# Kernel tuning notes

Measured on AMD Instinct MI355X. Metric: run time of the kernel, lower is better.

The kernel has to match this reference:

```python
import jax, jax.numpy as jnp
import numpy as np

NUM_CODES = 8192
CODE_DIM = 512
B, H, W = 16, 32, 32


def setup_inputs() -> dict:
    key = jax.random.key(0)
    k1, k2 = jax.random.split(key)
    z_e = jax.random.normal(k1, (B, H, W, CODE_DIM), dtype=jnp.float32)
    # variance_scaling(1.0, 'fan_in', 'uniform') ~ U(-sqrt(3/fan_in), sqrt(3/fan_in))
    lim = np.sqrt(3.0 / CODE_DIM)
    codebook = jax.random.uniform(k2, (NUM_CODES, CODE_DIM), dtype=jnp.float32,
                                  minval=-lim, maxval=lim)
    return {"z_e": z_e, "codebook": codebook}


def reference(z_e, codebook):
    shape = z_e.shape
    num_codes, code_dim = codebook.shape
    flat = z_e.reshape(-1, code_dim)                       # [N, D]
    d = (jnp.sum(flat * flat, axis=1, keepdims=True)
         + jnp.sum(codebook * codebook, axis=1)
         - 2.0 * jnp.matmul(flat, codebook.T))             # [N, K]
    indices = jnp.argmin(d, axis=1)                        # [N]
    z_q = codebook[indices].reshape(shape)
    idx_out = indices.reshape(shape[:-1])
    commitment_loss = jnp.mean((jax.lax.stop_gradient(z_q) - z_e) ** 2)
    codebook_loss = jnp.mean((z_q - jax.lax.stop_gradient(z_e)) ** 2)
    z_q_st = z_e + jax.lax.stop_gradient(z_q - z_e)        # straight-through
    # perplexity: mean one-hot == normalized histogram (avoids NxK one-hot)
    n = flat.shape[0]
    counts = jnp.zeros((num_codes,), dtype=z_e.dtype).at[indices].add(1.0)
    avg_probs = counts / n
    perplexity = jnp.exp(-jnp.sum(avg_probs * jnp.log(avg_probs + 1e-10)))
    return (z_q_st, idx_out, commitment_loss, codebook_loss, perplexity)
```

## Files before the change

kernel.cpp:

```cpp
#include <hip/hip_runtime.h>


#define N_PTS   16384
#define DIM     512
#define K_CODES 8192
#define KB      512
#define NSPLIT  16
#define OUT0_N  (N_PTS * DIM)
#define NELEM_F (8388608.0f)
#define MARGIN  1.5e-2f

typedef _Float16 half8 __attribute__((ext_vector_type(8)));
typedef _Float16 f16x4 __attribute__((ext_vector_type(4)));
typedef float    f32x4 __attribute__((ext_vector_type(4)));

#define SZ_A3    (16384UL * 512 * 2)
#define SZ_B3    (8192UL * 512 * 2)
#define OFF_A3   0UL
#define OFF_B3   (OFF_A3 + SZ_A3)
#define OFF_CN   (OFF_B3 + SZ_B3)
#define OFF_PV1  (OFF_CN + 32768UL)
#define SZ_P     (16UL * 16384 * 4)
#define OFF_PI1  (OFF_PV1 + SZ_P)
#define OFF_PV2  (OFF_PI1 + SZ_P)
#define OFF_PI2  (OFF_PV2 + SZ_P)
#define OFF_PSUM (OFF_PI2 + SZ_P)
#define OFF_CNT  (OFF_PSUM + 65536UL)
#define WS_NEED  (OFF_CNT + 32768UL)

#define GLOAD_LDS16(g, l) \
    __builtin_amdgcn_global_load_lds( \
        (const __attribute__((address_space(1))) unsigned int*)(g), \
        (__attribute__((address_space(3))) unsigned int*)(l), 16, 0, 0)

__global__ __launch_bounds__(128) void prep_all(const float* __restrict__ z_e,
                                                const float* __restrict__ cb,
                                                _Float16* __restrict__ A3,
                                                _Float16* __restrict__ B3,
                                                float* __restrict__ cnorm,
                                                unsigned int* __restrict__ counts) {
    const int b = blockIdx.x;
    const int t = threadIdx.x;
    if (b < 64) counts[b * 128 + t] = 0u;
    if (b < N_PTS) {
        const long r = b;
        const int d = t * 4;
        const float4 v = *(const float4*)(z_e + r * DIM + d);
        f16x4 h;
        h[0] = (_Float16)v.x; h[1] = (_Float16)v.y;
        h[2] = (_Float16)v.z; h[3] = (_Float16)v.w;
        *(f16x4*)(A3 + r * 512 + d) = h;
    } else {
        const long r = b - N_PTS;
        const int d = t * 4;
        const float4 v = *(const float4*)(cb + r * DIM + d);
        f16x4 h;
        h[0] = (_Float16)v.x; h[1] = (_Float16)v.y;
        h[2] = (_Float16)v.z; h[3] = (_Float16)v.w;
        *(f16x4*)(B3 + r * 512 + d) = h;
        float s = v.x * v.x + v.y * v.y + v.z * v.z + v.w * v.w;
#pragma unroll
        for (int o = 32; o > 0; o >>= 1) s += __shfl_down(s, o, 64);
        __shared__ float red[2];
        if ((t & 63) == 0) red[t >> 6] = s;
        __syncthreads();
        if (t == 0) cnorm[r] = red[0] + red[1];
    }
}

__global__ __launch_bounds__(128) void cnorm_kernel(const float* __restrict__ cb,
                                                    float* __restrict__ cnorm) {
    const int k = blockIdx.x;
    const int t = threadIdx.x;
    const float4 v = *(const float4*)(cb + (size_t)k * DIM + t * 4);
    float s = v.x * v.x + v.y * v.y + v.z * v.z + v.w * v.w;
#pragma unroll
    for (int o = 32; o > 0; o >>= 1) s += __shfl_down(s, o, 64);
    __shared__ float red[2];
    if ((t & 63) == 0) red[t >> 6] = s;
    __syncthreads();
    if (t == 0) cnorm[k] = red[0] + red[1];
}

__global__ __launch_bounds__(256, 3) void score_kernel(
    const _Float16* __restrict__ A3, const _Float16* __restrict__ B3,
    const float* __restrict__ cnorm,
    float* __restrict__ pv1, int* __restrict__ pi1,
    float* __restrict__ pv2, int* __restrict__ pi2) {
    __shared__ _Float16 As[128 * 64];
    __shared__ _Float16 Bs[128 * 64];
    __shared__ float mv1[128][2], mv2[128][2];
    __shared__ int   mj1[128][2], mj2[128][2];

    const int tid = threadIdx.x;
    const int w = tid >> 6;
    const int l = tid & 63;
    const int pbase = blockIdx.x * 128;
    const int nsplit = blockIdx.y;
    const int wmb = (w >> 1) * 64;
    const int wnb = (w & 1) * 64;
    const int srow = w * 8 + (l >> 3);
    const int scolh = (((l & 7) ^ ((l >> 3) & 7)) * 8);

    const _Float16* aB[4];
    const _Float16* bR[4];
#pragma unroll
    for (int it = 0; it < 4; ++it) {
        aB[it] = A3 + (long)(pbase + it * 32 + srow) * 512 + scolh;
        bR[it] = B3 + (long)(it * 32 + srow) * 512 + scolh;
    }

    const int q = l >> 4, x7 = l & 7, m16 = l & 15;
    const int koff0 = ((q ^ x7) * 8);
    const int rowAf = (wmb + m16) * 64;
    const int rowBf = (wnb + m16) * 64;

    float v1[16], v2[16];
    int i12[16];
#pragma unroll
    for (int s = 0; s < 16; ++s) { v1[s] = 3.0e38f; v2[s] = 3.0e38f; i12[s] = 0; }

#pragma unroll 1
    for (int nt = 0; nt < 4; ++nt) {
        const int kbase = nsplit * 512 + nt * 128;
        const long bOff = (long)kbase * 512;
        f32x4 acc[4][4];
#pragma unroll
        for (int mi = 0; mi < 4; ++mi)
#pragma unroll
            for (int ni = 0; ni < 4; ++ni)
                acc[mi][ni] = (f32x4){0.f, 0.f, 0.f, 0.f};

#pragma unroll 1
        for (int kt = 0; kt < KB / 64; ++kt) {
            const long ka = (long)kt * 64;
            __syncthreads();
#pragma unroll
            for (int it = 0; it < 4; ++it)
                GLOAD_LDS16(aB[it] + ka, &As[it * 2048 + w * 512]);
#pragma unroll
            for (int it = 0; it < 4; ++it)
                GLOAD_LDS16(bR[it] + bOff + ka, &Bs[it * 2048 + w * 512]);
            __syncthreads();
#pragma unroll
            for (int ks = 0; ks < 2; ++ks) {
                const int ko = koff0 ^ (ks * 32);
                half8 af[4], bf[4];
#pragma unroll
                for (int mi = 0; mi < 4; ++mi)
                    af[mi] = *(half8*)&As[rowAf + mi * 1024 + ko];
#pragma unroll
                for (int ni = 0; ni < 4; ++ni)
                    bf[ni] = *(half8*)&Bs[rowBf + ni * 1024 + ko];
#pragma unroll
                for (int mi = 0; mi < 4; ++mi)
#pragma unroll
                    for (int ni = 0; ni < 4; ++ni)
                        acc[mi][ni] = __builtin_amdgcn_mfma_f32_16x16x32_f16(
                            af[mi], bf[ni], acc[mi][ni], 0, 0, 0);
            }
        }
#pragma unroll
        for (int ni = 0; ni < 4; ++ni) {
            const int k = kbase + wnb + ni * 16 + m16;
            const float cn = cnorm[k];
#pragma unroll
            for (int mi = 0; mi < 4; ++mi)
#pragma unroll
                for (int r = 0; r < 4; ++r) {
                    const float s = fmaf(-2.0f, acc[mi][ni][r], cn);
                    const int slot = mi * 4 + r;
                    if (s < v1[slot]) {
                        v2[slot] = v1[slot];
                        i12[slot] = (k << 16) | (i12[slot] >> 16);
                        v1[slot] = s;
                    } else if (s < v2[slot]) {
                        v2[slot] = s;
                        i12[slot] = (i12[slot] & 0xffff0000) | k;
                    }
                }
        }
    }

#pragma unroll
    for (int slot = 0; slot < 16; ++slot) {
        float a1 = v1[slot], a2 = v2[slot];
        int b1 = i12[slot] >> 16, b2 = i12[slot] & 0xffff;
#pragma unroll
        for (int m = 1; m < 16; m <<= 1) {
            const float c1 = __shfl_xor(a1, m, 64);
            const int   d1 = __shfl_xor(b1, m, 64);
            const float c2 = __shfl_xor(a2, m, 64);
            const int   d2 = __shfl_xor(b2, m, 64);
            if (c1 < a1 || (c1 == a1 && d1 < b1)) {
                if (a1 < c2 || (a1 == c2 && b1 < d2)) { a2 = a1; b2 = b1; }
                else { a2 = c2; b2 = d2; }
                a1 = c1; b1 = d1;
            } else {
                if (c1 < a2 || (c1 == a2 && d1 < b2)) { a2 = c1; b2 = d1; }
            }
        }
        if ((l & 15) == 0) {
            const int sm = slot >> 2, sr = slot & 3;
            const int pr = wmb + sm * 16 + (l >> 4) * 4 + sr;
            const int h = w & 1;
            mv1[pr][h] = a1; mj1[pr][h] = b1;
            mv2[pr][h] = a2; mj2[pr][h] = b2;
        }
    }
    __syncthreads();
    if (tid < 128) {
        float a1 = mv1[tid][0], a2 = mv2[tid][0];
        int b1 = mj1[tid][0], b2 = mj2[tid][0];
        const float c1 = mv1[tid][1], c2 = mv2[tid][1];
        const int   d1 = mj1[tid][1], d2 = mj2[tid][1];
        if (c1 < a1 || (c1 == a1 && d1 < b1)) {
            if (a1 < c2 || (a1 == c2 && b1 < d2)) { a2 = a1; b2 = b1; }
            else { a2 = c2; b2 = d2; }
            a1 = c1; b1 = d1;
        } else {
            if (c1 < a2 || (c1 == a2 && d1 < b2)) { a2 = c1; b2 = d1; }
        }
        const size_t o = (size_t)nsplit * N_PTS + pbase + tid;
        pv1[o] = a1; pi1[o] = b1; pv2[o] = a2; pi2[o] = b2;
    }
}

__global__ __launch_bounds__(128) void gather_kernel(
    const float* __restrict__ z_e, const float* __restrict__ cb,
    const float* __restrict__ pv1, const int* __restrict__ pi1,
    const float* __restrict__ pv2, const int* __restrict__ pi2,
    float* __restrict__ out_q, float* __restrict__ out_idx,
    unsigned int* __restrict__ counts, float* __restrict__ psums) {
    const int p = blockIdx.x;
    const int t = threadIdx.x;

    __shared__ float sv1[NSPLIT], sv2[NSPLIT];
    __shared__ int   si1[NSPLIT], si2[NSPLIT];
    if (t < NSPLIT) {
        const size_t o = (size_t)t * N_PTS + p;
        sv1[t] = pv1[o]; si1[t] = pi1[o];
        sv2[t] = pv2[o]; si2[t] = pi2[o];
    }
    __syncthreads();

    float bv = 3.0e38f; int bi = 0x7fffffff;
#pragma unroll
    for (int s = 0; s < NSPLIT; ++s) {
        const float v = sv1[s];
        const int i = si1[s];
        if (v < bv || (v == bv && i < bi)) { bv = v; bi = i; }
    }
    float second = 3.0e38f;
    int cand[8]; int nc = 1; cand[0] = bi;
#pragma unroll
    for (int s = 0; s < NSPLIT; ++s) {
        const float v = sv1[s];
        const int i = si1[s];
        const float w2 = sv2[s];
        const int j = si2[s];
        if (i != bi) {
            if (v < second) second = v;
            if (v <= bv + MARGIN && nc < 8) cand[nc++] = i;
        }
        if (j != bi) {
            if (w2 < second) second = w2;
            if (w2 <= bv + MARGIN && nc < 8) cand[nc++] = j;
        }
    }

    __shared__ double dred[2];
    if (second - bv <= MARGIN && nc > 1) {
        double bestv = 1.0e300; int besti = 0x7fffffff;
        for (int c = 0; c < nc; ++c) {
            const int k = cand[c];
            double part = 0.0;
#pragma unroll
            for (int j = 0; j < 4; ++j) {
                const int d = t * 4 + j;
                const double cv = (double)cb[(size_t)k * DIM + d];
                const double zv = (double)z_e[(size_t)p * DIM + d];
                part += cv * cv - 2.0 * zv * cv;
            }
#pragma unroll
            for (int o = 32; o > 0; o >>= 1) part += __shfl_down(part, o, 64);
            if ((t & 63) == 0) dred[t >> 6] = part;
            __syncthreads();
            const double s = dred[0] + dred[1];
            __syncthreads();
            if (s < bestv || (s == bestv && k < besti)) { bestv = s; besti = k; }
        }
        bi = besti;
    }

    const float4 z = *(const float4*)(z_e + (size_t)p * DIM + t * 4);
    const float4 c = *(const float4*)(cb + (size_t)bi * DIM + t * 4);
    float4 d, o;
    d.x = c.x - z.x; d.y = c.y - z.y; d.z = c.z - z.z; d.w = c.w - z.w;
    o.x = z.x + d.x; o.y = z.y + d.y; o.z = z.z + d.z; o.w = z.w + d.w;
    *(float4*)(out_q + (size_t)p * DIM + t * 4) = o;
    float ls = d.x * d.x + d.y * d.y + d.z * d.z + d.w * d.w;
#pragma unroll
    for (int off = 32; off > 0; off >>= 1) ls += __shfl_down(ls, off, 64);
    __shared__ float red[2];
    if ((t & 63) == 0) red[t >> 6] = ls;
    __syncthreads();
    if (t == 0) {
        psums[p] = red[0] + red[1];
        out_idx[p] = (float)bi;
        atomicAdd(&counts[bi], 1u);
    }
}

__global__ __launch_bounds__(256) void finalize_kernel(
    const unsigned int* __restrict__ counts, const float* __restrict__ psums,
    float* __restrict__ out_scalars) {
    const int t = threadIdx.x;
    float ent = 0.0f;
    for (int b = t; b < K_CODES; b += 256) {
        const float pr = (float)counts[b] * (1.0f / 16384.0f);
        ent += pr * logf(pr + 1e-10f);
    }
    float ss = 0.0f;
    for (int i = t; i < N_PTS; i += 256) ss += psums[i];
#pragma unroll
    for (int off = 32; off > 0; off >>= 1) {
        ent += __shfl_down(ent, off, 64);
        ss += __shfl_down(ss, off, 64);
    }
    __shared__ float re[4], rs[4];
    if ((t & 63) == 0) { re[t >> 6] = ent; rs[t >> 6] = ss; }
    __syncthreads();
    if (t == 0) {
        const float loss = (rs[0] + rs[1] + rs[2] + rs[3]) * (1.0f / NELEM_F);
        out_scalars[0] = loss;
        out_scalars[1] = loss;
        out_scalars[2] = expf(-(re[0] + re[1] + re[2] + re[3]));
    }
}

#define FB_SPLIT 4
#define FB_KS    (K_CODES / FB_SPLIT)
#define FB_MT    128
#define FB_KT    128
#define FB_DT    32
#define FB_PITCH 36

__global__ __launch_bounds__(256, 2) void fb_dist_argmin_kernel(
    const float* __restrict__ z_e, const float* __restrict__ cb,
    const float* __restrict__ cnorm,
    float* __restrict__ pmin, int* __restrict__ pidx) {
    __shared__ float xs[FB_MT * FB_PITCH];
    __shared__ float cs[FB_KT * FB_PITCH];
    const int tid = threadIdx.x;
    const int tx = tid & 15, ty = tid >> 4;
    const int pbase = blockIdx.x * FB_MT;
    const int kbase0 = blockIdx.y * FB_KS;
    const int scol = (tid & 7) * 4, srow0 = tid >> 3;
    float mn[8], acc[8][8];
    int mi[8];
#pragma unroll
    for (int i = 0; i < 8; ++i) { mn[i] = 3.0e38f; mi[i] = 0; }
    for (int kt = 0; kt < FB_KS / FB_KT; ++kt) {
        const int kbase = kbase0 + kt * FB_KT;
#pragma unroll
        for (int i = 0; i < 8; ++i)
#pragma unroll
            for (int j = 0; j < 8; ++j) acc[i][j] = 0.0f;
        for (int dc = 0; dc < DIM / FB_DT; ++dc) {
            const int dbase = dc * FB_DT;
            __syncthreads();
#pragma unroll
            for (int it = 0; it < 4; ++it) {
                const int row = srow0 + it * 32;
                *(float4*)(xs + row * FB_PITCH + scol) =
                    *(const float4*)(z_e + (size_t)(pbase + row) * DIM + dbase + scol);
                *(float4*)(cs + row * FB_PITCH + scol) =
                    *(const float4*)(cb + (size_t)(kbase + row) * DIM + dbase + scol);
            }
            __syncthreads();
#pragma unroll 2
            for (int dd = 0; dd < FB_DT; dd += 4) {
                float4 xv[8], cv[8];
#pragma unroll
                for (int i = 0; i < 8; ++i)
                    xv[i] = *(const float4*)(xs + (ty + 16 * i) * FB_PITCH + dd);
#pragma unroll
                for (int j = 0; j < 8; ++j)
                    cv[j] = *(const float4*)(cs + (tx + 16 * j) * FB_PITCH + dd);
#pragma unroll
                for (int i = 0; i < 8; ++i)
#pragma unroll
                    for (int j = 0; j < 8; ++j)
                        acc[i][j] += xv[i].x * cv[j].x + xv[i].y * cv[j].y +
                                     xv[i].z * cv[j].z + xv[i].w * cv[j].w;
            }
        }
#pragma unroll
        for (int j = 0; j < 8; ++j) {
            const int k = kbase + tx + 16 * j;
            const float cn = cnorm[k];
#pragma unroll
            for (int i = 0; i < 8; ++i) {
                const float s = cn - 2.0f * acc[i][j];
                if (s < mn[i]) { mn[i] = s; mi[i] = k; }
            }
        }
    }
    float* rmin = xs;
    int* ridx = (int*)cs;
    __syncthreads();
#pragma unroll
    for (int i = 0; i < 8; ++i) {
        const int p = ty + 16 * i;
        rmin[p * 16 + tx] = mn[i];
        ridx[p * 16 + tx] = mi[i];
    }
    __syncthreads();
    if (tid < FB_MT) {
        float best = rmin[tid * 16];
        int bi = ridx[tid * 16];
#pragma unroll
        for (int t = 1; t < 16; ++t) {
            const float v = rmin[tid * 16 + t];
            const int k2 = ridx[tid * 16 + t];
            if (v < best || (v == best && k2 < bi)) { best = v; bi = k2; }
        }
        pmin[(size_t)blockIdx.y * N_PTS + pbase + tid] = best;
        pidx[(size_t)blockIdx.y * N_PTS + pbase + tid] = bi;
    }
}

__global__ __launch_bounds__(128) void fb_gather_kernel(
    const float* __restrict__ z_e, const float* __restrict__ cb,
    const float* __restrict__ pmin, const int* __restrict__ pidx,
    float* __restrict__ out_q, float* __restrict__ out_idx,
    unsigned int* __restrict__ counts, float* __restrict__ psums) {
    const int p = blockIdx.x;
    const int t = threadIdx.x;
    float best = pmin[p];
    int bi = pidx[p];
#pragma unroll
    for (int s = 1; s < FB_SPLIT; ++s) {
        const float v = pmin[(size_t)s * N_PTS + p];
        const int k2 = pidx[(size_t)s * N_PTS + p];
        if (v < best || (v == best && k2 < bi)) { best = v; bi = k2; }
    }
    const float4 z = *(const float4*)(z_e + (size_t)p * DIM + t * 4);
    const float4 c = *(const float4*)(cb + (size_t)bi * DIM + t * 4);
    float4 d, o;
    d.x = c.x - z.x; d.y = c.y - z.y; d.z = c.z - z.z; d.w = c.w - z.w;
    o.x = z.x + d.x; o.y = z.y + d.y; o.z = z.z + d.z; o.w = z.w + d.w;
    *(float4*)(out_q + (size_t)p * DIM + t * 4) = o;
    float ls = d.x * d.x + d.y * d.y + d.z * d.z + d.w * d.w;
#pragma unroll
    for (int off = 32; off > 0; off >>= 1) ls += __shfl_down(ls, off, 64);
    __shared__ float red[2];
    if ((t & 63) == 0) red[t >> 6] = ls;
    __syncthreads();
    if (t == 0) {
        psums[p] = red[0] + red[1];
        out_idx[p] = (float)bi;
        atomicAdd(&counts[bi], 1u);
    }
}

extern "C" void kernel_launch(void* const* d_in, const int* in_sizes, int n_in,
                              void* d_out, int out_size, void* d_ws, size_t ws_size,
                              hipStream_t stream) {
    const float* z_e = (const float*)d_in[0];
    const float* cb  = (const float*)d_in[1];
    float* out = (float*)d_out;
    char* ws = (char*)d_ws;

    if (ws_size >= WS_NEED) {
        _Float16* A3      = (_Float16*)(ws + OFF_A3);
        _Float16* B3      = (_Float16*)(ws + OFF_B3);
        float* cnorm      = (float*)(ws + OFF_CN);
        float* pv1        = (float*)(ws + OFF_PV1);
        int* pi1          = (int*)(ws + OFF_PI1);
        float* pv2        = (float*)(ws + OFF_PV2);
        int* pi2          = (int*)(ws + OFF_PI2);
        float* psums      = (float*)(ws + OFF_PSUM);
        unsigned int* cnt = (unsigned int*)(ws + OFF_CNT);

        prep_all<<<N_PTS + K_CODES, 128, 0, stream>>>(z_e, cb, A3, B3, cnorm, cnt);
        dim3 g(N_PTS / 128, NSPLIT);
        score_kernel<<<g, 256, 0, stream>>>(A3, B3, cnorm, pv1, pi1, pv2, pi2);
        gather_kernel<<<N_PTS, 128, 0, stream>>>(z_e, cb, pv1, pi1, pv2, pi2,
                                                 out, out + OUT0_N, cnt, psums);
        finalize_kernel<<<1, 256, 0, stream>>>(cnt, psums, out + OUT0_N + N_PTS);
    } else {
        float* cnorm      = (float*)ws;
        float* pmin       = (float*)(ws + 32768);
        int* pidx         = (int*)(ws + 32768 + 262144);
        unsigned int* cnt = (unsigned int*)(ws + 32768 + 2 * 262144);
        float* psums      = (float*)(ws + 32768 + 2 * 262144 + 32768);

        hipMemsetAsync(cnt, 0, 32768, stream);
        cnorm_kernel<<<K_CODES, 128, 0, stream>>>(cb, cnorm);
        dim3 grid1(N_PTS / FB_MT, FB_SPLIT);
        fb_dist_argmin_kernel<<<grid1, 256, 0, stream>>>(z_e, cb, cnorm, pmin, pidx);
        fb_gather_kernel<<<N_PTS, 128, 0, stream>>>(z_e, cb, pmin, pidx,
                                                    out, out + OUT0_N, cnt, psums);
        finalize_kernel<<<1, 256, 0, stream>>>(cnt, psums, out + OUT0_N + N_PTS);
    }
}
```

Measured before the change: 368.2 us.

## Rewrite score GEMM as 256x256 double-buffered, phase-interleaved MFMA pipeline

The fp16 distance GEMM moves from 128x128 tiles with 256 threads and single-buffered LDS to 256x256 tiles with 512 threads and a 128 KB double-buffered LDS. Global-to-LDS loads for the next K step are split across four compute phases, with explicit vmcnt waits, barriers and setprio around the MFMA bursts. The aim is to hide load latency behind compute and to raise data reuse per tile. The top-2 argmin is reduced per 256-code tile across lanes and waves, then merged into a running result. The large shared-memory footprint limits occupancy, and the hand-written waitcnt and barrier schedule is fragile.

```diff
diff --git a/kernel.cpp b/kernel.cpp
--- a/kernel.cpp
+++ b/kernel.cpp
@@ -4,7 +4,6 @@
 #define N_PTS   16384
 #define DIM     512
 #define K_CODES 8192
-#define KB      512
 #define NSPLIT  16
 #define OUT0_N  (N_PTS * DIM)
 #define NELEM_F (8388608.0f)
@@ -82,148 +81,188 @@
     if (t == 0) cnorm[k] = red[0] + red[1];
 }
 
-__global__ __launch_bounds__(256, 3) void score_kernel(
+__device__ __forceinline__ void top2_merge(float& a1, int& b1, float& a2, int& b2,
+                                           const float c1, const int d1,
+                                           const float c2, const int d2) {
+    if (c1 < a1 || (c1 == a1 && d1 < b1)) {
+        if (a1 < c2 || (a1 == c2 && b1 < d2)) { a2 = a1; b2 = b1; }
+        else { a2 = c2; b2 = d2; }
+        a1 = c1; b1 = d1;
+    } else {
+        if (c1 < a2 || (c1 == a2 && d1 < b2)) { a2 = c1; b2 = d1; }
+    }
+}
+
+__global__ __launch_bounds__(512, 2) void score_kernel(
     const _Float16* __restrict__ A3, const _Float16* __restrict__ B3,
     const float* __restrict__ cnorm,
     float* __restrict__ pv1, int* __restrict__ pi1,
     float* __restrict__ pv2, int* __restrict__ pi2) {
-    __shared__ _Float16 As[128 * 64];
-    __shared__ _Float16 Bs[128 * 64];
-    __shared__ float mv1[128][2], mv2[128][2];
-    __shared__ int   mj1[128][2], mj2[128][2];
+    __shared__ _Float16 smem[65536];
 
     const int tid = threadIdx.x;
-    const int w = tid >> 6;
-    const int l = tid & 63;
-    const int pbase = blockIdx.x * 128;
+    const int w   = tid >> 6;
+    const int l   = tid & 63;
+    const int wm  = w >> 2;
+    const int wn  = w & 3;
+    const int m16 = l & 15;
+    const int qq  = l >> 4;
+    const int x7  = l & 7;
+    const int pbase  = blockIdx.x * 256;
     const int nsplit = blockIdx.y;
-    const int wmb = (w >> 1) * 64;
-    const int wnb = (w & 1) * 64;
-    const int srow = w * 8 + (l >> 3);
-    const int scolh = (((l & 7) ^ ((l >> 3) & 7)) * 8);
-
-    const _Float16* aB[4];
-    const _Float16* bR[4];
-#pragma unroll
-    for (int it = 0; it < 4; ++it) {
-        aB[it] = A3 + (long)(pbase + it * 32 + srow) * 512 + scolh;
-        bR[it] = B3 + (long)(it * 32 + srow) * 512 + scolh;
-    }
-
-    const int q = l >> 4, x7 = l & 7, m16 = l & 15;
-    const int koff0 = ((q ^ x7) * 8);
-    const int rowAf = (wmb + m16) * 64;
-    const int rowBf = (wnb + m16) * 64;
-
-    float v1[16], v2[16];
-    int i12[16];
-#pragma unroll
-    for (int s = 0; s < 16; ++s) { v1[s] = 3.0e38f; v2[s] = 3.0e38f; i12[s] = 0; }
+
+    const int srow = tid >> 3;
+    const int sc   = ((tid & 7) ^ (srow & 7)) * 8;
+    const _Float16* gA = A3 + (size_t)(pbase + srow) * 512 + sc;
+
+    const int rA = wm * 128 + m16;
+    const int rB = wn * 64  + m16;
+    const int k0 = (qq ^ x7) * 8;
+
+#define STAGE_A(q, tau) \
+    GLOAD_LDS16(gA + (q) * 64 * 512 + (tau) * 64, \
+                &smem[(((tau) & 1) * 32768) + (q) * 4096 + w * 512])
+#define STAGE_B(q, tau) \
+    GLOAD_LDS16(gB + (q) * 64 * 512 + (tau) * 64, \
+                &smem[(((tau) & 1) * 32768) + 16384 + (q) * 4096 + w * 512])
+
+#define PHASE(mh, nh, STAGE_STMT, VM_STMT) do {                                 \
+    half8 af[4][2]; half8 bf[2][2];                                             \
+    _Pragma("unroll")                                                           \
+    for (int i_ = 0; i_ < 4; ++i_) {                                            \
+        const int r_ = (rA + ((mh) * 4 + i_) * 16) * 64;                        \
+        af[i_][0] = *(const half8*)&smem[bufo + r_ + k0];                       \
+        af[i_][1] = *(const half8*)&smem[bufo + r_ + (k0 ^ 32)];                \
+    }                                                                           \
+    _Pragma("unroll")                                                           \
+    for (int j_ = 0; j_ < 2; ++j_) {                                            \
+        const int r_ = (rB + ((nh) * 2 + j_) * 16) * 64;                        \
+        bf[j_][0] = *(const half8*)&smem[bufo + 16384 + r_ + k0];               \
+        bf[j_][1] = *(const half8*)&smem[bufo + 16384 + r_ + (k0 ^ 32)];        \
+    }                                                                           \
+    STAGE_STMT;                                                                 \
+    __builtin_amdgcn_s_barrier();                                               \
+    asm volatile("s_waitcnt lgkmcnt(0)" ::: "memory");                          \
+    __builtin_amdgcn_sched_barrier(0);                                          \
+    __builtin_amdgcn_s_setprio(1);                                              \
+    _Pragma("unroll")                                                           \
+    for (int i_ = 0; i_ < 4; ++i_)                                              \
+        _Pragma("unroll")                                                       \
+        for (int j_ = 0; j_ < 2; ++j_) {                                        \
+            acc[(mh) * 4 + i_][(nh) * 2 + j_] =                                 \
+                __builtin_amdgcn_mfma_f32_16x16x32_f16(                         \
+                    af[i_][0], bf[j_][0], acc[(mh) * 4 + i_][(nh) * 2 + j_],    \
+                    0, 0, 0);                                                   \
+            acc[(mh) * 4 + i_][(nh) * 2 + j_] =                                 \
+                __builtin_amdgcn_mfma_f32_16x16x32_f16(                         \
+                    af[i_][1], bf[j_][1], acc[(mh) * 4 + i_][(nh) * 2 + j_],    \
+                    0, 0, 0);                                                   \
+        }                                                                       \
+    __builtin_amdgcn_s_setprio(0);                                              \
+    VM_STMT;                                                                    \
+    __builtin_amdgcn_s_barrier();                                               \
+    __builtin_amdgcn_sched_barrier(0);                                          \
+} while (0)
+
+    float rv1 = 3.0e38f, rv2 = 3.0e38f;
+    int   ri1 = 0x7fffffff, ri2 = 0x7fffffff;
+
+    float* sc1 = (float*)smem;
+    float* sc2 = sc1 + 1024;
+    int*   si1 = (int*)(sc2 + 1024);
+    int*   si2 = si1 + 1024;
 
 #pragma unroll 1
-    for (int nt = 0; nt < 4; ++nt) {
-        const int kbase = nsplit * 512 + nt * 128;
-        const long bOff = (long)kbase * 512;
-        f32x4 acc[4][4];
-#pragma unroll
-        for (int mi = 0; mi < 4; ++mi)
+    for (int nt = 0; nt < 2; ++nt) {
+        const int kbase = nsplit * 512 + nt * 256;
+        const _Float16* gB = B3 + (size_t)(kbase + srow) * 512 + sc;
+
+        f32x4 acc[8][4];
+#pragma unroll
+        for (int mi = 0; mi < 8; ++mi)
 #pragma unroll
             for (int ni = 0; ni < 4; ++ni)
                 acc[mi][ni] = (f32x4){0.f, 0.f, 0.f, 0.f};
 
+        STAGE_A(0, 0); STAGE_A(2, 0); STAGE_A(1, 0); STAGE_A(3, 0);
+        STAGE_B(0, 0); STAGE_B(1, 0); STAGE_B(2, 0); STAGE_B(3, 0);
+        STAGE_A(0, 1); STAGE_A(2, 1);
+        asm volatile("s_waitcnt vmcnt(2)" ::: "memory");
+        __builtin_amdgcn_s_barrier();
+        __builtin_amdgcn_sched_barrier(0);
+
 #pragma unroll 1
-        for (int kt = 0; kt < KB / 64; ++kt) {
-            const long ka = (long)kt * 64;
-            __syncthreads();
-#pragma unroll
-            for (int it = 0; it < 4; ++it)
-                GLOAD_LDS16(aB[it] + ka, &As[it * 2048 + w * 512]);
-#pragma unroll
-            for (int it = 0; it < 4; ++it)
-                GLOAD_LDS16(bR[it] + bOff + ka, &Bs[it * 2048 + w * 512]);
-            __syncthreads();
-#pragma unroll
-            for (int ks = 0; ks < 2; ++ks) {
-                const int ko = koff0 ^ (ks * 32);
-                half8 af[4], bf[4];
-#pragma unroll
-                for (int mi = 0; mi < 4; ++mi)
-                    af[mi] = *(half8*)&As[rowAf + mi * 1024 + ko];
-#pragma unroll
-                for (int ni = 0; ni < 4; ++ni)
-                    bf[ni] = *(half8*)&Bs[rowBf + ni * 1024 + ko];
-#pragma unroll
-                for (int mi = 0; mi < 4; ++mi)
-#pragma unroll
-                    for (int ni = 0; ni < 4; ++ni)
-                        acc[mi][ni] = __builtin_amdgcn_mfma_f32_16x16x32_f16(
-                            af[mi], bf[ni], acc[mi][ni], 0, 0, 0);
+        for (int g = 0; g < 8; ++g) {
+            const int bufo = (g & 1) * 32768;
+            PHASE(0, 0,
+                  { if (g < 7) { STAGE_A(1, g + 1); STAGE_A(3, g + 1); } },
+                  {});
+            PHASE(0, 1,
+                  { if (g < 7) { STAGE_B(0, g + 1); STAGE_B(1, g + 1); } },
+                  {});
+            PHASE(1, 0,
+                  { if (g < 7) { STAGE_B(2, g + 1); STAGE_B(3, g + 1); } },
+                  {});
+            PHASE(1, 1,
+                  { if (g < 6) { STAGE_A(0, g + 2); STAGE_A(2, g + 2); } },
+                  { if (g < 6) asm volatile("s_waitcnt vmcnt(2)" ::: "memory");
+                    else if (g == 6) asm volatile("s_waitcnt vmcnt(0)" ::: "memory"); });
+        }
+
+        const int kb2 = kbase + wn * 64;
+        float cn[4];
+#pragma unroll
+        for (int ni = 0; ni < 4; ++ni) cn[ni] = cnorm[kb2 + ni * 16 + m16];
+
+#pragma unroll
+        for (int mi = 0; mi < 8; ++mi) {
+#pragma unroll
+            for (int r = 0; r < 4; ++r) {
+                float a1 = 3.0e38f, a2 = 3.0e38f;
+                int   b1 = 0x7fffffff, b2 = 0x7fffffff;
+#pragma unroll
+                for (int ni = 0; ni < 4; ++ni) {
+                    const float s = fmaf(-2.0f, acc[mi][ni][r], cn[ni]);
+                    const int k = kb2 + ni * 16 + m16;
+                    if (s < a1) { a2 = a1; b2 = b1; a1 = s; b1 = k; }
+                    else if (s < a2) { a2 = s; b2 = k; }
+                }
+#pragma unroll
+                for (int m = 1; m < 16; m <<= 1) {
+                    const float c1 = __shfl_xor(a1, m, 64);
+                    const int   d1 = __shfl_xor(b1, m, 64);
+                    const float c2 = __shfl_xor(a2, m, 64);
+                    const int   d2 = __shfl_xor(b2, m, 64);
+                    top2_merge(a1, b1, a2, b2, c1, d1, c2, d2);
+                }
+                if ((l & 15) == 0) {
+                    const int pr = wm * 128 + mi * 16 + qq * 4 + r;
+                    sc1[pr * 4 + wn] = a1; si1[pr * 4 + wn] = b1;
+                    sc2[pr * 4 + wn] = a2; si2[pr * 4 + wn] = b2;
+                }
             }
         }
-#pragma unroll
-        for (int ni = 0; ni < 4; ++ni) {
-            const int k = kbase + wnb + ni * 16 + m16;
-            const float cn = cnorm[k];
-#pragma unroll
-            for (int mi = 0; mi < 4; ++mi)
-#pragma unroll
-                for (int r = 0; r < 4; ++r) {
-                    const float s = fmaf(-2.0f, acc[mi][ni][r], cn);
-                    const int slot = mi * 4 + r;
-                    if (s < v1[slot]) {
-                        v2[slot] = v1[slot];
-                        i12[slot] = (k << 16) | (i12[slot] >> 16);
-                        v1[slot] = s;
-                    } else if (s < v2[slot]) {
-                        v2[slot] = s;
-                        i12[slot] = (i12[slot] & 0xffff0000) | k;
-                    }
-                }
-        }
-    }
-
-#pragma unroll
-    for (int slot = 0; slot < 16; ++slot) {
-        float a1 = v1[slot], a2 = v2[slot];
-        int b1 = i12[slot] >> 16, b2 = i12[slot] & 0xffff;
-#pragma unroll
-        for (int m = 1; m < 16; m <<= 1) {
-            const float c1 = __shfl_xor(a1, m, 64);
-            const int   d1 = __shfl_xor(b1, m, 64);
-            const float c2 = __shfl_xor(a2, m, 64);
-            const int   d2 = __shfl_xor(b2, m, 64);
-            if (c1 < a1 || (c1 == a1 && d1 < b1)) {
-                if (a1 < c2 || (a1 == c2 && b1 < d2)) { a2 = a1; b2 = b1; }
-                else { a2 = c2; b2 = d2; }
-                a1 = c1; b1 = d1;
-            } else {
-                if (c1 < a2 || (c1 == a2 && d1 < b2)) { a2 = c1; b2 = d1; }
-            }
-        }
-        if ((l & 15) == 0) {
-            const int sm = slot >> 2, sr = slot & 3;
-            const int pr = wmb + sm * 16 + (l >> 4) * 4 + sr;
-            const int h = w & 1;
-            mv1[pr][h] = a1; mj1[pr][h] = b1;
-            mv2[pr][h] = a2; mj2[pr][h] = b2;
-        }
-    }
-    __syncthreads();
-    if (tid < 128) {
-        float a1 = mv1[tid][0], a2 = mv2[tid][0];
-        int b1 = mj1[tid][0], b2 = mj2[tid][0];
-        const float c1 = mv1[tid][1], c2 = mv2[tid][1];
-        const int   d1 = mj1[tid][1], d2 = mj2[tid][1];
-        if (c1 < a1 || (c1 == a1 && d1 < b1)) {
-            if (a1 < c2 || (a1 == c2 && b1 < d2)) { a2 = a1; b2 = b1; }
-            else { a2 = c2; b2 = d2; }
-            a1 = c1; b1 = d1;
-        } else {
-            if (c1 < a2 || (c1 == a2 && d1 < b2)) { a2 = c1; b2 = d1; }
-        }
+        __syncthreads();
+        if (tid < 256) {
+            float a1 = sc1[tid * 4], a2 = sc2[tid * 4];
+            int   b1 = si1[tid * 4], b2 = si2[tid * 4];
+#pragma unroll
+            for (int gg = 1; gg < 4; ++gg)
+                top2_merge(a1, b1, a2, b2, sc1[tid * 4 + gg], si1[tid * 4 + gg],
+                           sc2[tid * 4 + gg], si2[tid * 4 + gg]);
+            top2_merge(rv1, ri1, rv2, ri2, a1, b1, a2, b2);
+        }
+        __syncthreads();
+    }
+
+    if (tid < 256) {
         const size_t o = (size_t)nsplit * N_PTS + pbase + tid;
-        pv1[o] = a1; pi1[o] = b1; pv2[o] = a2; pi2[o] = b2;
-    }
+        pv1[o] = rv1; pi1[o] = ri1;
+        pv2[o] = rv2; pi2[o] = ri2;
+    }
+#undef STAGE_A
+#undef STAGE_B
+#undef PHASE
 }
 
 __global__ __launch_bounds__(128) void gather_kernel(
@@ -485,8 +524,8 @@
         unsigned int* cnt = (unsigned int*)(ws + OFF_CNT);
 
         prep_all<<<N_PTS + K_CODES, 128, 0, stream>>>(z_e, cb, A3, B3, cnorm, cnt);
-        dim3 g(N_PTS / 128, NSPLIT);
-        score_kernel<<<g, 256, 0, stream>>>(A3, B3, cnorm, pv1, pi1, pv2, pi2);
+        dim3 g(N_PTS / 256, NSPLIT);
+        score_kernel<<<g, 512, 0, stream>>>(A3, B3, cnorm, pv1, pi1, pv2, pi2);
         gather_kernel<<<N_PTS, 128, 0, stream>>>(z_e, cb, pv1, pi1, pv2, pi2,
                                                  out, out + OUT0_N, cnt, psums);
         finalize_kernel<<<1, 256, 0, stream>>>(cnt, psums, out + OUT0_N + N_PTS);
```

After: 761.5 us. 107% more time.
